# Kernel optimization log

Hardware: AMD Instinct MI355X
Metric: run time of the kernel (lower is better)

Reference implementation:

```python
import jax, jax.numpy as jnp
import numpy as np


def setup_inputs() -> dict:
    key = jax.random.key(0)
    k1, k2 = jax.random.split(key)
    X1 = jax.random.normal(k1, (1024, 64, 128), dtype=jnp.float32)
    X2 = jax.random.normal(k2, (1024, 64, 128), dtype=jnp.float32)
    return {"X1": X1, "X2": X2}


def reference(X1, X2):
    # Y[n, m, t] = mean_d (X1[n, t, d] - X2[m, t, d])^2
    # O(N*M*T*D) broadcast intermediate; same math as the Keras layer.
    D = X1.shape[-1]
    x1_sq = jnp.sum(X1 * X1, axis=-1)  # [N, T]
    x2_sq = jnp.sum(X2 * X2, axis=-1)  # [M, T]
    cross = jnp.einsum('ntd,mtd->nmt', X1, X2)  # [N, M, T] via GEMM
    Y = (x1_sq[:, None, :] - 2.0 * cross + x2_sq[None, :, :]) / D
    return Y
```

## Files before the change

### kernel.cpp

```cpp
#include <hip/hip_runtime.h>
#include <stdint.h>


#define NN 1024
#define MM 1024
#define TT 64
#define DD 128

typedef _Float16 f16x8 __attribute__((ext_vector_type(8)));
typedef float f32x4 __attribute__((ext_vector_type(4)));
typedef float f32x2 __attribute__((ext_vector_type(2)));

#define X1H_OFF 0u
#define X2H_OFF (16u << 20)
#define N1_OFF  (32u << 20)
#define N2_OFF  ((32u << 20) + (256u << 10))
#define WS_NEED ((size_t)(32u << 20) + (512u << 10))

__global__ __launch_bounds__(256) void prep_kernel(
    const float* __restrict__ X1, const float* __restrict__ X2,
    uint32_t* __restrict__ ws)
{
    const int lane = threadIdx.x & 63;
    const int wv   = threadIdx.x >> 6;
    const int gid  = blockIdx.x * 4 + wv;
    const int src  = gid >> 16;
    const int rem  = gid & 65535;
    const int n    = rem >> 6;
    const int t    = rem & 63;

    const float* X  = src ? X2 : X1;
    uint32_t* Xh    = ws + ((src ? X2H_OFF : X1H_OFF) >> 2);
    float*    nrm   = (float*)ws + ((src ? N2_OFF : N1_OFF) >> 2);

    f32x2 v = *(const f32x2*)&X[((size_t)n * TT + t) * DD + lane * 2];
    float s = v[0]*v[0] + v[1]*v[1];
    union { uint32_t u; _Float16 h[2]; } pk;
    pk.h[0] = (_Float16)v[0]; pk.h[1] = (_Float16)v[1];
    Xh[(size_t)(t * NN + n) * 64 + (lane ^ ((n & 7) << 2))] = pk.u;

    s += __shfl_xor(s, 1);  s += __shfl_xor(s, 2);  s += __shfl_xor(s, 4);
    s += __shfl_xor(s, 8);  s += __shfl_xor(s, 16); s += __shfl_xor(s, 32);
    if (lane == 0) nrm[n * TT + t] = s;
}

#define STAGE(ts_, p_) do {                                                  \
    const char* ga_ = aA + ((size_t)(ts_) << 18);                            \
    const char* gb_ = aB + ((size_t)(ts_) << 18);                            \
    __builtin_amdgcn_global_load_lds(                                        \
        (const __attribute__((address_space(1))) void*)ga_,                  \
        (__attribute__((address_space(3))) void*)&As[p_][wv << 10], 16,0,0); \
    __builtin_amdgcn_global_load_lds(                                        \
        (const __attribute__((address_space(1))) void*)(ga_ + 1024),         \
        (__attribute__((address_space(3))) void*)&As[p_][(wv<<10)+512],16,0,0);\
    __builtin_amdgcn_global_load_lds(                                        \
        (const __attribute__((address_space(1))) void*)gb_,                  \
        (__attribute__((address_space(3))) void*)&Bs[p_][wv << 9], 16,0,0);  \
} while (0)

__global__ __launch_bounds__(512, 4) void sim_kernel(
    const uint32_t* __restrict__ wsu, float* __restrict__ Y)
{
    __shared__ _Float16 As[2][64 * 128];
    __shared__ _Float16 Bs[2][32 * 128];

    const int b    = blockIdx.x;
    const int wgid = (b & 7) * 256 + (b >> 3);
    const int tg   = wgid >> 9;
    const int c    = wgid & 511;
    const int n0   = (c >> 5) << 6;
    const int m0   = (c & 31) << 5;
    const int t0   = tg << 4;

    const int tid  = threadIdx.x;
    const int lane = tid & 63;
    const int wv   = tid >> 6;
    const int q = lane >> 4, r = lane & 15;
    const int wn = wv >> 1, wm = wv & 1;

    const char* wsb = (const char*)wsu;
    const char* aA = wsb + X1H_OFF + ((size_t)(t0 * NN + n0) << 8)
                   + (wv << 11) + (lane << 4);
    const char* aB = wsb + X2H_OFF + ((size_t)(t0 * NN + m0) << 8)
                   + (wv << 10) + (lane << 4);

    f32x4 acc[16];
    #pragma unroll
    for (int i = 0; i < 16; ++i) acc[i] = (f32x4){0.f, 0.f, 0.f, 0.f};

    const int arow = wn * 16 + r;
    const int brow = wm * 16 + r;
    const int ah   = (arow & 7) << 3;
    const int bh   = (brow & 7) << 3;
    const int fcol = q * 8;

    STAGE(0, 0);

    #pragma unroll
    for (int ts = 0; ts < 16; ++ts) {
        const int p = ts & 1;
        if (ts < 15) {
            STAGE(ts + 1, p ^ 1);
            asm volatile("s_waitcnt vmcnt(3)" ::: "memory");
        } else {
            asm volatile("s_waitcnt vmcnt(0)" ::: "memory");
        }
        __builtin_amdgcn_s_barrier();
        asm volatile("" ::: "memory");

        #pragma unroll
        for (int kc = 0; kc < 4; ++kc) {
            f16x8 af = *(const f16x8*)&As[p][arow * 128 + ((kc*32 + fcol) ^ ah)];
            f16x8 bf = *(const f16x8*)&Bs[p][brow * 128 + ((kc*32 + fcol) ^ bh)];
            acc[ts] = __builtin_amdgcn_mfma_f32_16x16x32_f16(af, bf, acc[ts], 0, 0, 0);
        }

        if (ts < 15) {
            asm volatile("" ::: "memory");
            __builtin_amdgcn_s_barrier();
        }
    }

    const float* n1 = (const float*)(wsb + N1_OFF);
    const float* n2 = (const float*)(wsb + N2_OFF);
    const int m = m0 + wm * 16 + r;
    f32x4 bn4[4];
    {
        const float* p2 = &n2[(size_t)m * TT + t0];
        #pragma unroll
        for (int tq = 0; tq < 4; ++tq) bn4[tq] = ((const f32x4*)p2)[tq];
    }
    const float inv = 1.0f / 128.0f;
    #pragma unroll
    for (int rr = 0; rr < 4; ++rr) {
        const int n = n0 + wn * 16 + q * 4 + rr;
        const float* p1 = &n1[(size_t)n * TT + t0];
        f32x4 an4[4];
        #pragma unroll
        for (int tq = 0; tq < 4; ++tq) an4[tq] = ((const f32x4*)p1)[tq];
        float* yb = Y + ((size_t)n * MM + m) * TT + t0;
        #pragma unroll
        for (int tq = 0; tq < 4; ++tq) {
            f32x4 o;
            #pragma unroll
            for (int e = 0; e < 4; ++e)
                o[e] = (an4[tq][e] + bn4[tq][e] - 2.0f * acc[tq*4 + e][rr]) * inv;
            ((f32x4*)yb)[tq] = o;
        }
    }
}

#define LDA 132
#define LDN 17

__global__ __launch_bounds__(512, 4) void sim_kernel_fb(
    const float* __restrict__ X1, const float* __restrict__ X2,
    float* __restrict__ Y)
{
    __shared__ _Float16 As[2][64 * LDA];
    __shared__ _Float16 Bs[2][32 * LDA];
    __shared__ float an[64 * LDN];
    __shared__ float bn[32 * LDN];

    const int b   = blockIdx.x;
    const int clo = b & 7;
    const int tg  = (b >> 3) & 3;
    const int chi = b >> 5;
    const int c   = (chi << 3) | clo;
    const int n0  = (c >> 5) << 6;
    const int m0  = (c & 31) << 5;
    const int t0  = tg << 4;

    const int tid  = threadIdx.x;
    const int lane = tid & 63;
    const int wave = tid >> 6;
    const int q = lane >> 4, r = lane & 15;
    const int wn = wave >> 1, wm = wave & 1;

    const int arow = tid >> 3;
    const int acol = (tid & 7) << 4;
    const int brow = tid >> 4;
    const int bcol = (tid & 15) << 3;

    const float* pA = X1 + ((size_t)(n0 + arow) * TT + t0) * DD + acol;
    const float* pB = X2 + ((size_t)(m0 + brow) * TT + t0) * DD + bcol;

    f32x4 acc[16];
    #pragma unroll
    for (int i = 0; i < 16; ++i) acc[i] = (f32x4){0.f, 0.f, 0.f, 0.f};

    f32x4 uA[4];
    f32x4 uB[2];
    uA[0] = ((const f32x4*)pA)[0]; uA[1] = ((const f32x4*)pA)[1];
    uA[2] = ((const f32x4*)pA)[2]; uA[3] = ((const f32x4*)pA)[3];
    uB[0] = ((const f32x4*)pB)[0]; uB[1] = ((const f32x4*)pB)[1];

    #pragma unroll
    for (int tl = 0; tl < 16; ++tl) {
        _Float16* __restrict__ Abuf = As[tl & 1];
        _Float16* __restrict__ Bbuf = Bs[tl & 1];

        float sA = 0.f;
        #pragma unroll
        for (int j = 0; j < 4; ++j)
            sA += uA[j][0]*uA[j][0] + uA[j][1]*uA[j][1]
                + uA[j][2]*uA[j][2] + uA[j][3]*uA[j][3];
        f16x8 hA0, hA1;
        #pragma unroll
        for (int e = 0; e < 4; ++e) { hA0[e] = (_Float16)uA[0][e]; hA0[e+4] = (_Float16)uA[1][e]; }
        #pragma unroll
        for (int e = 0; e < 4; ++e) { hA1[e] = (_Float16)uA[2][e]; hA1[e+4] = (_Float16)uA[3][e]; }
        sA += __shfl_xor(sA, 1); sA += __shfl_xor(sA, 2); sA += __shfl_xor(sA, 4);

        float sB = uB[0][0]*uB[0][0] + uB[0][1]*uB[0][1]
                 + uB[0][2]*uB[0][2] + uB[0][3]*uB[0][3]
                 + uB[1][0]*uB[1][0] + uB[1][1]*uB[1][1]
                 + uB[1][2]*uB[1][2] + uB[1][3]*uB[1][3];
        f16x8 hB;
        #pragma unroll
        for (int e = 0; e < 4; ++e) { hB[e] = (_Float16)uB[0][e]; hB[e+4] = (_Float16)uB[1][e]; }
        sB += __shfl_xor(sB, 1); sB += __shfl_xor(sB, 2);
        sB += __shfl_xor(sB, 4); sB += __shfl_xor(sB, 8);

        *(f16x8*)&Abuf[arow * LDA + acol]     = hA0;
        *(f16x8*)&Abuf[arow * LDA + acol + 8] = hA1;
        *(f16x8*)&Bbuf[brow * LDA + bcol]     = hB;
        if ((tid & 7)  == 0) an[arow * LDN + tl] = sA;
        if ((tid & 15) == 0) bn[brow * LDN + tl] = sB;

        __syncthreads();

        if (tl < 15) {
            const float* nA = pA + (size_t)(tl + 1) * DD;
            const float* nB = pB + (size_t)(tl + 1) * DD;
            uA[0] = ((const f32x4*)nA)[0]; uA[1] = ((const f32x4*)nA)[1];
            uA[2] = ((const f32x4*)nA)[2]; uA[3] = ((const f32x4*)nA)[3];
            uB[0] = ((const f32x4*)nB)[0]; uB[1] = ((const f32x4*)nB)[1];
        }

        #pragma unroll
        for (int kc = 0; kc < 4; ++kc) {
            f16x8 af = *(const f16x8*)&Abuf[(wn*16 + r) * LDA + kc*32 + q*8];
            f16x8 bf = *(const f16x8*)&Bbuf[(wm*16 + r) * LDA + kc*32 + q*8];
            acc[tl] = __builtin_amdgcn_mfma_f32_16x16x32_f16(af, bf, acc[tl], 0, 0, 0);
        }
    }

    float bnv[16];
    {
        const float* pb = &bn[(wm*16 + r) * LDN];
        #pragma unroll
        for (int e = 0; e < 16; ++e) bnv[e] = pb[e];
    }
    const float inv = 1.0f / 128.0f;
    #pragma unroll
    for (int rr = 0; rr < 4; ++rr) {
        const float* pa = &an[(wn*16 + q*4 + rr) * LDN];
        float anv[16];
        #pragma unroll
        for (int e = 0; e < 16; ++e) anv[e] = pa[e];
        const size_t n = (size_t)(n0 + wn*16 + q*4 + rr);
        const size_t m = (size_t)(m0 + wm*16 + r);
        float* yb = Y + (n * MM + m) * TT + t0;
        #pragma unroll
        for (int tq = 0; tq < 4; ++tq) {
            f32x4 o;
            #pragma unroll
            for (int e = 0; e < 4; ++e) {
                const int tl = tq*4 + e;
                o[e] = (anv[tl] + bnv[tl] - 2.0f * acc[tl][rr]) * inv;
            }
            ((f32x4*)yb)[tq] = o;
        }
    }
}

extern "C" void kernel_launch(void* const* d_in, const int* in_sizes, int n_in,
                              void* d_out, int out_size, void* d_ws, size_t ws_size,
                              hipStream_t stream) {
    const float* X1 = (const float*)d_in[0];
    const float* X2 = (const float*)d_in[1];
    float* Y = (float*)d_out;
    if (d_ws != nullptr && ws_size >= WS_NEED) {
        prep_kernel<<<dim3(32768), dim3(256), 0, stream>>>(X1, X2, (uint32_t*)d_ws);
        sim_kernel<<<dim3(2048), dim3(512), 0, stream>>>((const uint32_t*)d_ws, Y);
    } else {
        sim_kernel_fb<<<dim3(2048), dim3(512), 0, stream>>>(X1, X2, Y);
    }
}
```

Measured before the change: 456.0 us.

## Triple-buffer A tiles, single barrier per step, and widen prep kernel loads

The prep kernel now has each wave convert 16 timesteps of one row with 128-bit loads and 64-bit stores, replacing one wave per (n,t) pair. This cuts the launch from 32768 blocks to 2048. The sim kernel moves to a three-deep A buffer and a two-deep B buffer, issuing the next loads after a single barrier and dropping the trailing barrier. It also raises wave priority around the MFMA section. Tile indices are remapped into 8x8 groups for better L2 locality, at the cost of extra LDS and somewhat more complex wait-count reasoning.

```diff
diff --git a/kernel.cpp b/kernel.cpp
--- a/kernel.cpp
+++ b/kernel.cpp
@@ -9,7 +9,7 @@
 
 typedef _Float16 f16x8 __attribute__((ext_vector_type(8)));
 typedef float f32x4 __attribute__((ext_vector_type(4)));
-typedef float f32x2 __attribute__((ext_vector_type(2)));
+typedef uint32_t u32x2 __attribute__((ext_vector_type(2)));
 
 #define X1H_OFF 0u
 #define X2H_OFF (16u << 20)
@@ -24,35 +24,47 @@
     const int lane = threadIdx.x & 63;
     const int wv   = threadIdx.x >> 6;
     const int gid  = blockIdx.x * 4 + wv;
-    const int src  = gid >> 16;
-    const int rem  = gid & 65535;
-    const int n    = rem >> 6;
-    const int t    = rem & 63;
-
-    const float* X  = src ? X2 : X1;
-    uint32_t* Xh    = ws + ((src ? X2H_OFF : X1H_OFF) >> 2);
-    float*    nrm   = (float*)ws + ((src ? N2_OFF : N1_OFF) >> 2);
-
-    f32x2 v = *(const f32x2*)&X[((size_t)n * TT + t) * DD + lane * 2];
-    float s = v[0]*v[0] + v[1]*v[1];
-    union { uint32_t u; _Float16 h[2]; } pk;
-    pk.h[0] = (_Float16)v[0]; pk.h[1] = (_Float16)v[1];
-    Xh[(size_t)(t * NN + n) * 64 + (lane ^ ((n & 7) << 2))] = pk.u;
-
-    s += __shfl_xor(s, 1);  s += __shfl_xor(s, 2);  s += __shfl_xor(s, 4);
-    s += __shfl_xor(s, 8);  s += __shfl_xor(s, 16); s += __shfl_xor(s, 32);
-    if (lane == 0) nrm[n * TT + t] = s;
+    const int src  = gid >> 12;
+    const int rem  = gid & 4095;
+    const int n    = rem >> 2;
+    const int tq   = rem & 3;
+
+    const float* X = src ? X2 : X1;
+    uint32_t* Xh   = ws + ((src ? X2H_OFF : X1H_OFF) >> 2);
+    float*    nrm  = (float*)ws + ((src ? N2_OFF : N1_OFF) >> 2);
+
+    const int th  = lane >> 5;
+    const int l32 = lane & 31;
+    const int swz = (n & 7) << 2;
+
+    #pragma unroll
+    for (int i = 0; i < 8; ++i) {
+        const int t = tq * 16 + i * 2 + th;
+        f32x4 v = *(const f32x4*)&X[((size_t)n * TT + t) * DD + l32 * 4];
+        float s = v[0]*v[0] + v[1]*v[1] + v[2]*v[2] + v[3]*v[3];
+        union { u32x2 u2; uint32_t u[2]; _Float16 h[4]; } pk;
+        pk.h[0] = (_Float16)v[0]; pk.h[1] = (_Float16)v[1];
+        pk.h[2] = (_Float16)v[2]; pk.h[3] = (_Float16)v[3];
+        uint32_t* row = &Xh[(size_t)(t * NN + n) * 64];
+        *(u32x2*)&row[(l32 * 2) ^ swz] = pk.u2;
+
+        s += __shfl_xor(s, 1); s += __shfl_xor(s, 2); s += __shfl_xor(s, 4);
+        s += __shfl_xor(s, 8); s += __shfl_xor(s, 16);
+        if (l32 == 0) nrm[n * TT + t] = s;
+    }
 }
 
-#define STAGE(ts_, p_) do {                                                  \
+#define STAGE_A(ts_, p_) do {                                                \
     const char* ga_ = aA + ((size_t)(ts_) << 18);                            \
-    const char* gb_ = aB + ((size_t)(ts_) << 18);                            \
     __builtin_amdgcn_global_load_lds(                                        \
         (const __attribute__((address_space(1))) void*)ga_,                  \
         (__attribute__((address_space(3))) void*)&As[p_][wv << 10], 16,0,0); \
     __builtin_amdgcn_global_load_lds(                                        \
         (const __attribute__((address_space(1))) void*)(ga_ + 1024),         \
         (__attribute__((address_space(3))) void*)&As[p_][(wv<<10)+512],16,0,0);\
+} while (0)
+#define STAGE_B(ts_, p_) do {                                                \
+    const char* gb_ = aB + ((size_t)(ts_) << 18);                            \
     __builtin_amdgcn_global_load_lds(                                        \
         (const __attribute__((address_space(1))) void*)gb_,                  \
         (__attribute__((address_space(3))) void*)&Bs[p_][wv << 9], 16,0,0);  \
@@ -61,15 +73,17 @@
 __global__ __launch_bounds__(512, 4) void sim_kernel(
     const uint32_t* __restrict__ wsu, float* __restrict__ Y)
 {
-    __shared__ _Float16 As[2][64 * 128];
+    __shared__ _Float16 As[3][64 * 128];
     __shared__ _Float16 Bs[2][32 * 128];
 
     const int b    = blockIdx.x;
     const int wgid = (b & 7) * 256 + (b >> 3);
     const int tg   = wgid >> 9;
     const int c    = wgid & 511;
-    const int n0   = (c >> 5) << 6;
-    const int m0   = (c & 31) << 5;
+    const int nt   = ((c >> 8) << 3) | ((c >> 3) & 7);
+    const int mt   = (((c >> 6) & 3) << 3) | (c & 7);
+    const int n0   = nt << 6;
+    const int m0   = mt << 5;
     const int t0   = tg << 4;
 
     const int tid  = threadIdx.x;
@@ -94,31 +108,29 @@
     const int bh   = (brow & 7) << 3;
     const int fcol = q * 8;
 
-    STAGE(0, 0);
+    STAGE_A(0, 0);
+    STAGE_B(0, 0);
+    STAGE_A(1, 1);
 
     #pragma unroll
     for (int ts = 0; ts < 16; ++ts) {
-        const int p = ts & 1;
-        if (ts < 15) {
-            STAGE(ts + 1, p ^ 1);
-            asm volatile("s_waitcnt vmcnt(3)" ::: "memory");
-        } else {
-            asm volatile("s_waitcnt vmcnt(0)" ::: "memory");
-        }
+        const int pa = ts % 3, pb = ts & 1;
+        if (ts < 15) asm volatile("s_waitcnt vmcnt(2)" ::: "memory");
+        else         asm volatile("s_waitcnt vmcnt(0)" ::: "memory");
         __builtin_amdgcn_s_barrier();
         asm volatile("" ::: "memory");
 
+        if (ts < 15) STAGE_B(ts + 1, (ts + 1) & 1);
+        if (ts < 14) STAGE_A(ts + 2, (ts + 2) % 3);
+
+        __builtin_amdgcn_s_setprio(1);
         #pragma unroll
         for (int kc = 0; kc < 4; ++kc) {
-            f16x8 af = *(const f16x8*)&As[p][arow * 128 + ((kc*32 + fcol) ^ ah)];
-            f16x8 bf = *(const f16x8*)&Bs[p][brow * 128 + ((kc*32 + fcol) ^ bh)];
+            f16x8 af = *(const f16x8*)&As[pa][arow * 128 + ((kc*32 + fcol) ^ ah)];
+            f16x8 bf = *(const f16x8*)&Bs[pb][brow * 128 + ((kc*32 + fcol) ^ bh)];
             acc[ts] = __builtin_amdgcn_mfma_f32_16x16x32_f16(af, bf, acc[ts], 0, 0, 0);
         }
-
-        if (ts < 15) {
-            asm volatile("" ::: "memory");
-            __builtin_amdgcn_s_barrier();
-        }
+        __builtin_amdgcn_s_setprio(0);
     }
 
     const float* n1 = (const float*)(wsb + N1_OFF);
@@ -157,8 +169,8 @@
     const float* __restrict__ X1, const float* __restrict__ X2,
     float* __restrict__ Y)
 {
-    __shared__ _Float16 As[2][64 * LDA];
-    __shared__ _Float16 Bs[2][32 * LDA];
+    __shared__ _Float16 Asf[2][64 * LDA];
+    __shared__ _Float16 Bsf[2][32 * LDA];
     __shared__ float an[64 * LDN];
     __shared__ float bn[32 * LDN];
 
@@ -197,8 +209,8 @@
 
     #pragma unroll
     for (int tl = 0; tl < 16; ++tl) {
-        _Float16* __restrict__ Abuf = As[tl & 1];
-        _Float16* __restrict__ Bbuf = Bs[tl & 1];
+        _Float16* __restrict__ Abuf = Asf[tl & 1];
+        _Float16* __restrict__ Bbuf = Bsf[tl & 1];
 
         float sA = 0.f;
         #pragma unroll
@@ -282,7 +294,7 @@
     const float* X2 = (const float*)d_in[1];
     float* Y = (float*)d_out;
     if (d_ws != nullptr && ws_size >= WS_NEED) {
-        prep_kernel<<<dim3(32768), dim3(256), 0, stream>>>(X1, X2, (uint32_t*)d_ws);
+        prep_kernel<<<dim3(2048), dim3(256), 0, stream>>>(X1, X2, (uint32_t*)d_ws);
         sim_kernel<<<dim3(2048), dim3(512), 0, stream>>>((const uint32_t*)d_ws, Y);
     } else {
         sim_kernel_fb<<<dim3(2048), dim3(512), 0, stream>>>(X1, X2, Y);
```

After: 457.8 us. Within noise of the previous version (+0.4%).
